# Kernel optimization log

Hardware: AMD Instinct MI355X
Metric: run time of the kernel (lower is better)

## Reference

```python
import jax, jax.numpy as jnp
import numpy as np

N_NODES = 100000
N_EDGES = 1600000
IN_CH = 128
HID = 128
OUT_CH = 16
N_GRAPHS = 64


def setup_inputs() -> dict:
    key = jax.random.key(0)
    ks = jax.random.split(key, 8)
    x = jax.random.normal(ks[0], (N_NODES, IN_CH), dtype=jnp.float32)
    edge_index = jax.random.randint(ks[1], (2, N_EDGES), 0, N_NODES, dtype=jnp.int64)
    batch = jnp.sort(jax.random.randint(ks[2], (N_NODES,), 0, N_GRAPHS, dtype=jnp.int64))
    s1 = 1.0 / np.sqrt(IN_CH)
    s2 = 1.0 / np.sqrt(HID)
    W1 = jax.random.uniform(ks[3], (IN_CH, HID), jnp.float32, -s1, s1)
    b1 = jnp.zeros((HID,), jnp.float32)
    W2 = jax.random.uniform(ks[4], (HID, HID), jnp.float32, -s2, s2)
    b2 = jnp.zeros((HID,), jnp.float32)
    Wfc = jax.random.uniform(ks[5], (HID, OUT_CH), jnp.float32, -s2, s2)
    bfc = jax.random.uniform(ks[6], (OUT_CH,), jnp.float32, -s2, s2)
    return {"x": x, "W1": W1, "b1": b1, "W2": W2, "b2": b2,
            "Wfc": Wfc, "bfc": bfc, "edge_index": edge_index, "batch": batch}


def _gcn_conv(x, W, b, src, dst, deg_inv_sqrt, deg_inv):
    # GCNConv with self-loops: out = D^-1/2 (A+I) D^-1/2 (x W) + b
    h = x @ W                                   # [N, H]
    norm = deg_inv_sqrt[src] * deg_inv_sqrt[dst]  # [E]
    agg = jax.ops.segment_sum(h[src] * norm[:, None], dst, num_segments=N_NODES)
    # self-loop term: deg_inv_sqrt[i]^2 * h[i]
    return agg + h * deg_inv[:, None] + b


def reference(x, W1, b1, W2, b2, Wfc, bfc, edge_index, batch):
    src, dst = edge_index[0], edge_index[1]
    # degree including self-loop
    deg = jax.ops.segment_sum(jnp.ones((N_EDGES,), jnp.float32), dst, num_segments=N_NODES) + 1.0
    deg_inv_sqrt = jax.lax.rsqrt(deg)
    deg_inv = 1.0 / deg
    h = jax.nn.relu(_gcn_conv(x, W1, b1, src, dst, deg_inv_sqrt, deg_inv))
    h = jax.nn.relu(_gcn_conv(h, W2, b2, src, dst, deg_inv_sqrt, deg_inv))
    # global mean pool over graphs
    sums = jax.ops.segment_sum(h, batch, num_segments=N_GRAPHS)          # [G, H]
    counts = jax.ops.segment_sum(jnp.ones((N_NODES,), jnp.float32), batch, num_segments=N_GRAPHS)
    pooled = sums / jnp.maximum(counts, 1.0)[:, None]
    return pooled @ Wfc + bfc
```

## Files before the change

### kernel.cpp

```cpp
#include <hip/hip_runtime.h>
#include <math.h>

#define NN 100000
#define NE 1600000
#define CH 128
#define OUTC 16
#define NG 64

#define CBSH 8
#define NCB 391
#define CHK 4096
#define HCHK 8192
#define HISTB 196
#define PREPB 391
#define MAXB 6144
#define PS 8
#define LDA 136

typedef __attribute__((ext_vector_type(8))) short bf16x8;
typedef __attribute__((ext_vector_type(4))) float f32x4;

__device__ __forceinline__ unsigned short f2bf(float f) {
    union { float f; unsigned u; } v; v.f = f;
    unsigned r = v.u + 0x7FFF + ((v.u >> 16) & 1);
    return (unsigned short)(r >> 16);
}
__device__ __forceinline__ float bflo(unsigned u) {
    union { unsigned u; float f; } v; v.u = u << 16; return v.f;
}
__device__ __forceinline__ float bfhi(unsigned u) {
    union { unsigned u; float f; } v; v.u = u & 0xffff0000u; return v.f;
}

__global__ __launch_bounds__(256) void k_fused0(const int* __restrict__ edst, int* __restrict__ bcnt,
                         const float* __restrict__ W2, unsigned short* __restrict__ wt2,
                         const int* __restrict__ batch, int* __restrict__ gptr,
                         int* __restrict__ gfill, float* __restrict__ pooled) {
    int b = blockIdx.x;
    int t = threadIdx.x;
    if (b < HISTB) {
        __shared__ int h[NCB];
        for (int i = t; i < NCB; i += 256) h[i] = 0;
        __syncthreads();
        int base = b * HCHK;
#pragma unroll
        for (int i = 0; i < 32; i++) {
            int e = base + i * 256 + t;
            if (e < NE) atomicAdd(&h[edst[e] >> CBSH], 1);
        }
        __syncthreads();
        for (int i = t; i < NCB; i += 256)
            if (h[i]) atomicAdd(&bcnt[i], h[i]);
    } else {
        int i = (b - HISTB) * 256 + t;
        if (i < CH * CH) {
            int k = i >> 7, n = i & 127;
            wt2[n * CH + k] = f2bf(W2[i]);
        }
        if (i < NCB) gfill[i] = 0;
        if (i < NG * CH) pooled[i] = 0.f;
        if (i < NN) {
            int bb = batch[i];
            int prev = (i == 0) ? -1 : batch[i - 1];
            for (int g = prev + 1; g <= bb; g++) gptr[g] = i;
            if (i == NN - 1) {
                for (int g = bb + 1; g <= NG; g++) gptr[g] = NN;
            }
        }
    }
}

__global__ __launch_bounds__(512) void k_passA(const int* __restrict__ src, const int* __restrict__ dst,
                        const int* __restrict__ bcnt, int* __restrict__ gfill,
                        unsigned* __restrict__ ebuf, int* __restrict__ ebase) {
    __shared__ unsigned lbuf[CHK];
    __shared__ unsigned short lbkt[CHK];
    __shared__ int hcnt[NCB];
    __shared__ int hbase[512];
    __shared__ int eb[512];
    __shared__ int goff[NCB];
    int t = threadIdx.x;
    for (int i = t; i < NCB; i += 512) hcnt[i] = 0;
    eb[t] = (t < NCB) ? bcnt[t] : 0;
    __syncthreads();
    int base = blockIdx.x * CHK;
    int cb[8], slot[8]; unsigned pk[8];
#pragma unroll
    for (int i = 0; i < 8; i++) {
        int e = base + i * 512 + t;
        cb[i] = -1;
        if (e < NE) {
            int d = dst[e], s = src[e];
            cb[i] = d >> CBSH;
            pk[i] = ((unsigned)s << CBSH) | (unsigned)(d & 255);
            slot[i] = atomicAdd(&hcnt[cb[i]], 1);
        }
    }
    __syncthreads();
    hbase[t] = (t < NCB) ? hcnt[t] : 0;
    __syncthreads();
    for (int off = 1; off < 512; off <<= 1) {
        int v1 = 0, v2 = 0;
        if (t >= off) { v1 = hbase[t - off]; v2 = eb[t - off]; }
        __syncthreads();
        if (t >= off) { hbase[t] += v1; eb[t] += v2; }
        __syncthreads();
    }
    if (t < NCB) {
        int c = hcnt[t];
        int g = c ? atomicAdd(&gfill[t], c) : 0;
        int eb_ex = t ? eb[t - 1] : 0;
        goff[t] = eb_ex + g - (hbase[t] - c);
    }
    if (blockIdx.x == 0) {
        if (t == 0) ebase[0] = 0;
        if (t < NCB) ebase[t + 1] = eb[t];
    }
    __syncthreads();
#pragma unroll
    for (int i = 0; i < 8; i++) {
        if (cb[i] >= 0) {
            int pos = hbase[cb[i]] - hcnt[cb[i]] + slot[i];
            lbuf[pos] = pk[i];
            lbkt[pos] = (unsigned short)cb[i];
        }
    }
    __syncthreads();
    int total = min(NE - base, CHK);
    for (int p = t; p < total; p += 512) {
        unsigned v = lbuf[p];
        int bk = lbkt[p];
        ebuf[goff[bk] + p] = v;
    }
}

__launch_bounds__(256, 2)
__global__ void k_fusedB(const unsigned* __restrict__ ebuf, const int* __restrict__ ebase,
                         int* __restrict__ degi, int* __restrict__ rowst,
                         float* __restrict__ dis, int* __restrict__ csr,
                         const float* __restrict__ x, const float* __restrict__ W1,
                         unsigned short* __restrict__ bufA) {
    __shared__ __align__(16) unsigned short smem[128 * LDA];
    int b = blockIdx.x;
    int t = threadIdx.x;

    if (b < NCB) {
        int* cnt   = (int*)smem;
        int* nbase = cnt + 256;
        int* fill  = nbase + 256;
        int* stage = fill + 256;
        int cb = b;
        int nb0 = cb << CBSH;
        int ncnt = min(256, NN - nb0);
        int e0 = ebase[cb], e1 = ebase[cb + 1];
        cnt[t] = 0; fill[t] = 0;
        __syncthreads();
        for (int e = e0 + t; e < e1; e += 256)
            atomicAdd(&cnt[ebuf[e] & 255], 1);
        __syncthreads();
        nbase[t] = cnt[t];
        __syncthreads();
        for (int off = 1; off < 256; off <<= 1) {
            int v = 0;
            if (t >= off) v = nbase[t - off];
            __syncthreads();
            if (t >= off) nbase[t] += v;
            __syncthreads();
        }
        for (int e = e0 + t; e < e1; e += 256) {
            unsigned v = ebuf[e];
            int local = v & 255;
            int s = atomicAdd(&fill[local], 1);
            stage[nbase[local] - cnt[local] + s] = (int)(v >> CBSH);
        }
        __syncthreads();
        int total = e1 - e0;
        for (int p = t; p < total; p += 256) csr[e0 + p] = stage[p];
        if (t < ncnt) {
            int c = cnt[t];
            degi[nb0 + t] = c;
            rowst[nb0 + t] = e0 + nbase[t] - c;
            dis[nb0 + t] = rsqrtf((float)c + 1.0f);
        }
    } else {
        unsigned short* wlds = smem;
#pragma unroll
        for (int it = 0; it < 64; it++) {
            int i = it * 256 + t;
            int k = i >> 7, n = i & 127;
            wlds[n * LDA + k] = f2bf(W1[i]);
        }
        __syncthreads();

        int wave = t >> 6, lane = t & 63;
        int quad = lane >> 4, l16 = lane & 15;
        int rbase = (b - NCB) * 128 + wave * 32;

        bf16x8 af[2][4];
#pragma unroll
        for (int s = 0; s < 2; s++) {
            int row = rbase + s * 16 + l16;
            if (row >= NN) row = NN - 1;
            const float* arow = x + (size_t)row * CH + quad * 8;
#pragma unroll
            for (int ks = 0; ks < 4; ks++) {
                float4 lo = *(const float4*)(arow + ks * 32);
                float4 hi = *(const float4*)(arow + ks * 32 + 4);
                union { bf16x8 v; unsigned short u[8]; } tmp;
                tmp.u[0] = f2bf(lo.x); tmp.u[1] = f2bf(lo.y);
                tmp.u[2] = f2bf(lo.z); tmp.u[3] = f2bf(lo.w);
                tmp.u[4] = f2bf(hi.x); tmp.u[5] = f2bf(hi.y);
                tmp.u[6] = f2bf(hi.z); tmp.u[7] = f2bf(hi.w);
                af[s][ks] = tmp.v;
            }
        }

        f32x4 acc[2][8];
#pragma unroll
        for (int s = 0; s < 2; s++)
#pragma unroll
            for (int tt = 0; tt < 8; tt++) acc[s][tt] = (f32x4){0.f, 0.f, 0.f, 0.f};

#pragma unroll
        for (int tt = 0; tt < 8; tt++) {
            const unsigned short* wcol = &wlds[(tt * 16 + l16) * LDA + quad * 8];
            bf16x8 b0 = *(const bf16x8*)(wcol);
            bf16x8 b1 = *(const bf16x8*)(wcol + 32);
            bf16x8 b2 = *(const bf16x8*)(wcol + 64);
            bf16x8 b3 = *(const bf16x8*)(wcol + 96);
#pragma unroll
            for (int s = 0; s < 2; s++) {
                acc[s][tt] = __builtin_amdgcn_mfma_f32_16x16x32_bf16(af[s][0], b0, acc[s][tt], 0, 0, 0);
                acc[s][tt] = __builtin_amdgcn_mfma_f32_16x16x32_bf16(af[s][1], b1, acc[s][tt], 0, 0, 0);
                acc[s][tt] = __builtin_amdgcn_mfma_f32_16x16x32_bf16(af[s][2], b2, acc[s][tt], 0, 0, 0);
                acc[s][tt] = __builtin_amdgcn_mfma_f32_16x16x32_bf16(af[s][3], b3, acc[s][tt], 0, 0, 0);
            }
        }

#pragma unroll
        for (int s = 0; s < 2; s++) {
#pragma unroll
            for (int r = 0; r < 4; r++) {
                int orow = rbase + s * 16 + quad * 4 + r;
                if (orow < NN) {
#pragma unroll
                    for (int tt = 0; tt < 8; tt++)
                        bufA[(size_t)orow * CH + tt * 16 + l16] = f2bf(acc[s][tt][r]);
                }
            }
        }
    }
}

__global__ __launch_bounds__(256) void k_agg_w(const unsigned short* __restrict__ ht, const int* __restrict__ rowst,
                      const int* __restrict__ degi, const int* __restrict__ csr,
                      const float* __restrict__ dis, const float* __restrict__ bias,
                      unsigned short* __restrict__ out) {
    int t = threadIdx.x;
    int grp = t >> 4;
    int q = t & 15;
    int n = blockIdx.x * 16 + grp;
    const uint4* base = (const uint4*)ht;

    float d = dis[n];
    uint4 sv = base[(size_t)n * 16 + q];
    float a[8];
    a[0] = d * bflo(sv.x); a[1] = d * bfhi(sv.x);
    a[2] = d * bflo(sv.y); a[3] = d * bfhi(sv.y);
    a[4] = d * bflo(sv.z); a[5] = d * bfhi(sv.z);
    a[6] = d * bflo(sv.w); a[7] = d * bfhi(sv.w);

    int start = rowst[n];
    int c = degi[n];
    int nb = c & ~7;
    int j = 0;
    for (; j < nb; j += 8) {
        int idx[8];
#pragma unroll
        for (int u = 0; u < 8; u++) idx[u] = csr[start + j + u];
        uint4 v[8]; float w[8];
#pragma unroll
        for (int u = 0; u < 8; u++) v[u] = base[(size_t)idx[u] * 16 + q];
#pragma unroll
        for (int u = 0; u < 8; u++) w[u] = dis[idx[u]];
#pragma unroll
        for (int u = 0; u < 8; u++) {
            a[0] = fmaf(w[u], bflo(v[u].x), a[0]); a[1] = fmaf(w[u], bfhi(v[u].x), a[1]);
            a[2] = fmaf(w[u], bflo(v[u].y), a[2]); a[3] = fmaf(w[u], bfhi(v[u].y), a[3]);
            a[4] = fmaf(w[u], bflo(v[u].z), a[4]); a[5] = fmaf(w[u], bfhi(v[u].z), a[5]);
            a[6] = fmaf(w[u], bflo(v[u].w), a[6]); a[7] = fmaf(w[u], bfhi(v[u].w), a[7]);
        }
    }
    if (j < c) {
        int idx[8];
#pragma unroll
        for (int u = 0; u < 8; u++) { int e = j + u; idx[u] = csr[start + (e < c ? e : c - 1)]; }
        uint4 v[8]; float w[8];
#pragma unroll
        for (int u = 0; u < 8; u++) v[u] = base[(size_t)idx[u] * 16 + q];
#pragma unroll
        for (int u = 0; u < 8; u++) w[u] = dis[idx[u]];
#pragma unroll
        for (int u = 0; u < 8; u++) {
            if (j + u < c) {
                a[0] = fmaf(w[u], bflo(v[u].x), a[0]); a[1] = fmaf(w[u], bfhi(v[u].x), a[1]);
                a[2] = fmaf(w[u], bflo(v[u].y), a[2]); a[3] = fmaf(w[u], bfhi(v[u].y), a[3]);
                a[4] = fmaf(w[u], bflo(v[u].z), a[4]); a[5] = fmaf(w[u], bfhi(v[u].z), a[5]);
                a[6] = fmaf(w[u], bflo(v[u].w), a[6]); a[7] = fmaf(w[u], bfhi(v[u].w), a[7]);
            }
        }
    }

    const float4* bp = (const float4*)bias;
    float4 b0 = bp[q * 2], b1 = bp[q * 2 + 1];
    uint4 o;
    {
        float ox = fmaxf(fmaf(d, a[0], b0.x), 0.f), oy = fmaxf(fmaf(d, a[1], b0.y), 0.f);
        o.x = ((unsigned)f2bf(oy) << 16) | (unsigned)f2bf(ox);
        ox = fmaxf(fmaf(d, a[2], b0.z), 0.f); oy = fmaxf(fmaf(d, a[3], b0.w), 0.f);
        o.y = ((unsigned)f2bf(oy) << 16) | (unsigned)f2bf(ox);
        ox = fmaxf(fmaf(d, a[4], b1.x), 0.f); oy = fmaxf(fmaf(d, a[5], b1.y), 0.f);
        o.z = ((unsigned)f2bf(oy) << 16) | (unsigned)f2bf(ox);
        ox = fmaxf(fmaf(d, a[6], b1.z), 0.f); oy = fmaxf(fmaf(d, a[7], b1.w), 0.f);
        o.w = ((unsigned)f2bf(oy) << 16) | (unsigned)f2bf(ox);
    }
    ((uint4*)out)[(size_t)n * 16 + q] = o;
}

__launch_bounds__(256, 2)
__global__ void k_gemm2(const unsigned short* __restrict__ Av,
                        const unsigned short* __restrict__ WT,
                        const float* __restrict__ dis,
                        unsigned short* __restrict__ out) {
    int tid = threadIdx.x;
    int wave = tid >> 6, lane = tid & 63;
    int quad = lane >> 4, l16 = lane & 15;

    int rbase = blockIdx.x * 128 + wave * 32;

    bf16x8 af[2][4];
#pragma unroll
    for (int s = 0; s < 2; s++) {
        int row = rbase + s * 16 + l16;
        if (row >= NN) row = NN - 1;
        const unsigned short* arow = Av + (size_t)row * CH + quad * 8;
#pragma unroll
        for (int ks = 0; ks < 4; ks++) af[s][ks] = *(const bf16x8*)(arow + ks * 32);
    }

    f32x4 acc[2][8];
#pragma unroll
    for (int s = 0; s < 2; s++)
#pragma unroll
        for (int t = 0; t < 8; t++) acc[s][t] = (f32x4){0.f, 0.f, 0.f, 0.f};

#pragma unroll
    for (int t = 0; t < 8; t++) {
        const unsigned short* wcol = WT + (size_t)(t * 16 + l16) * CH + quad * 8;
        bf16x8 b0 = *(const bf16x8*)(wcol);
        bf16x8 b1 = *(const bf16x8*)(wcol + 32);
        bf16x8 b2 = *(const bf16x8*)(wcol + 64);
        bf16x8 b3 = *(const bf16x8*)(wcol + 96);
#pragma unroll
        for (int s = 0; s < 2; s++) {
            acc[s][t] = __builtin_amdgcn_mfma_f32_16x16x32_bf16(af[s][0], b0, acc[s][t], 0, 0, 0);
            acc[s][t] = __builtin_amdgcn_mfma_f32_16x16x32_bf16(af[s][1], b1, acc[s][t], 0, 0, 0);
            acc[s][t] = __builtin_amdgcn_mfma_f32_16x16x32_bf16(af[s][2], b2, acc[s][t], 0, 0, 0);
            acc[s][t] = __builtin_amdgcn_mfma_f32_16x16x32_bf16(af[s][3], b3, acc[s][t], 0, 0, 0);
        }
    }

#pragma unroll
    for (int s = 0; s < 2; s++) {
#pragma unroll
        for (int r = 0; r < 4; r++) {
            int orow = rbase + s * 16 + quad * 4 + r;
            if (orow < NN) {
                float d = dis[orow];
#pragma unroll
                for (int t = 0; t < 8; t++) {
                    out[(size_t)orow * CH + t * 16 + l16] = f2bf(acc[s][t][r] * d);
                }
            }
        }
    }
}

__global__ __launch_bounds__(256) void k_agg(const unsigned short* __restrict__ ht, const int* __restrict__ rowst,
                      const int* __restrict__ degi, const int* __restrict__ csr,
                      const float* __restrict__ dis, const float* __restrict__ bias,
                      unsigned short* __restrict__ out) {
    int t = threadIdx.x;
    int grp = t >> 4;
    int q = t & 15;
    int n = blockIdx.x * 16 + grp;
    const uint4* base = (const uint4*)ht;

    uint4 sv = base[(size_t)n * 16 + q];
    float a[8];
    a[0] = bflo(sv.x); a[1] = bfhi(sv.x);
    a[2] = bflo(sv.y); a[3] = bfhi(sv.y);
    a[4] = bflo(sv.z); a[5] = bfhi(sv.z);
    a[6] = bflo(sv.w); a[7] = bfhi(sv.w);

    int start = rowst[n];
    int c = degi[n];
    int nb = c & ~7;
    int j = 0;
    for (; j < nb; j += 8) {
        int idx[8];
#pragma unroll
        for (int u = 0; u < 8; u++) idx[u] = csr[start + j + u];
        uint4 v[8];
#pragma unroll
        for (int u = 0; u < 8; u++) v[u] = base[(size_t)idx[u] * 16 + q];
#pragma unroll
        for (int u = 0; u < 8; u++) {
            a[0] += bflo(v[u].x); a[1] += bfhi(v[u].x);
            a[2] += bflo(v[u].y); a[3] += bfhi(v[u].y);
            a[4] += bflo(v[u].z); a[5] += bfhi(v[u].z);
            a[6] += bflo(v[u].w); a[7] += bfhi(v[u].w);
        }
    }
    if (j < c) {
        int idx[8];
#pragma unroll
        for (int u = 0; u < 8; u++) { int e = j + u; idx[u] = csr[start + (e < c ? e : c - 1)]; }
        uint4 v[8];
#pragma unroll
        for (int u = 0; u < 8; u++) v[u] = base[(size_t)idx[u] * 16 + q];
#pragma unroll
        for (int u = 0; u < 8; u++) {
            if (j + u < c) {
                a[0] += bflo(v[u].x); a[1] += bfhi(v[u].x);
                a[2] += bflo(v[u].y); a[3] += bfhi(v[u].y);
                a[4] += bflo(v[u].z); a[5] += bfhi(v[u].z);
                a[6] += bflo(v[u].w); a[7] += bfhi(v[u].w);
            }
        }
    }

    float d = dis[n];
    const float4* bp = (const float4*)bias;
    float4 b0 = bp[q * 2], b1 = bp[q * 2 + 1];
    uint4 o;
    {
        float ox = fmaxf(fmaf(d, a[0], b0.x), 0.f), oy = fmaxf(fmaf(d, a[1], b0.y), 0.f);
        o.x = ((unsigned)f2bf(oy) << 16) | (unsigned)f2bf(ox);
        ox = fmaxf(fmaf(d, a[2], b0.z), 0.f); oy = fmaxf(fmaf(d, a[3], b0.w), 0.f);
        o.y = ((unsigned)f2bf(oy) << 16) | (unsigned)f2bf(ox);
        ox = fmaxf(fmaf(d, a[4], b1.x), 0.f); oy = fmaxf(fmaf(d, a[5], b1.y), 0.f);
        o.z = ((unsigned)f2bf(oy) << 16) | (unsigned)f2bf(ox);
        ox = fmaxf(fmaf(d, a[6], b1.z), 0.f); oy = fmaxf(fmaf(d, a[7], b1.w), 0.f);
        o.w = ((unsigned)f2bf(oy) << 16) | (unsigned)f2bf(ox);
    }
    ((uint4*)out)[(size_t)n * 16 + q] = o;
}

__global__ __launch_bounds__(512) void k_pool2(const unsigned short* __restrict__ h,
                                               const int* __restrict__ gptr,
                                               float* __restrict__ pooled) {
    int g = blockIdx.x >> 3;
    int s = blockIdx.x & 7;
    int gs = gptr[g], ge = gptr[g + 1];
    int len = ge - gs;
    int i0 = gs + (int)(((long long)len * s) >> 3);
    int i1 = gs + (int)(((long long)len * (s + 1)) >> 3);
    int t = threadIdx.x;
    int pr = t & 63;
    int ro = t >> 6;
    const unsigned* base = (const unsigned*)h;
    float s0 = 0.f, s1 = 0.f;
    for (int n = i0 + ro; n < i1; n += 8) {
        unsigned v = base[(size_t)n * 64 + pr];
        s0 += bflo(v); s1 += bfhi(v);
    }
    __shared__ float red[2][8][64];
    red[0][ro][pr] = s0; red[1][ro][pr] = s1;
    __syncthreads();
    for (int off = 4; off >= 1; off >>= 1) {
        if (ro < off) {
            red[0][ro][pr] += red[0][ro + off][pr];
            red[1][ro][pr] += red[1][ro + off][pr];
        }
        __syncthreads();
    }
    if (ro == 0) {
        atomicAdd(&pooled[g * CH + pr * 2],     red[0][0][pr]);
        atomicAdd(&pooled[g * CH + pr * 2 + 1], red[1][0][pr]);
    }
}

__global__ void k_final(const float* __restrict__ pooled, const int* __restrict__ gptr,
                        const float* __restrict__ Wfc, const float* __restrict__ bfc,
                        float* __restrict__ out) {
    int idx = blockIdx.x * 256 + threadIdx.x;
    if (idx >= NG * OUTC) return;
    int g = idx >> 4, o = idx & 15;
    float c = (float)(gptr[g + 1] - gptr[g]);
    float inv = 1.0f / fmaxf(c, 1.0f);
    float s = 0.f;
    for (int k = 0; k < CH; k++) s += pooled[g * CH + k] * Wfc[k * OUTC + o];
    out[idx] = fmaf(s, inv, bfc[o]);
}

extern "C" void kernel_launch(void* const* d_in, const int* in_sizes, int n_in,
                              void* d_out, int out_size, void* d_ws, size_t ws_size,
                              hipStream_t stream) {
    (void)in_sizes; (void)n_in; (void)out_size; (void)ws_size;
    const float* x   = (const float*)d_in[0];
    const float* W1  = (const float*)d_in[1];
    const float* b1  = (const float*)d_in[2];
    const float* W2  = (const float*)d_in[3];
    const float* b2  = (const float*)d_in[4];
    const float* Wfc = (const float*)d_in[5];
    const float* bfc = (const float*)d_in[6];
    const int* ei    = (const int*)d_in[7];
    const int* batch = (const int*)d_in[8];
    const int* esrc = ei;
    const int* edst = ei + NE;
    float* out = (float*)d_out;

    char* w = (char*)d_ws;
    unsigned short* bufA = (unsigned short*)w; w += (size_t)NN * CH * 2;
    unsigned short* bufB = (unsigned short*)w; w += (size_t)NN * CH * 2;
    unsigned short* wt2  = (unsigned short*)w; w += (size_t)CH * CH * 2;
    unsigned* ebuf = (unsigned*)w; w += (size_t)NE * 4;
    int* csr    = (int*)w;    w += (size_t)NE * 4;
    int* degi   = (int*)w;    w += (size_t)NN * 4;
    int* rowst  = (int*)w;    w += (size_t)NN * 4;
    float* dis  = (float*)w;  w += (size_t)NN * 4;
    int* bcnt   = (int*)w;    w += NCB * 4;
    int* ebase  = (int*)w;    w += (NCB + 1) * 4;
    int* gfill  = (int*)w;    w += NCB * 4;
    int* gptr   = (int*)w;    w += (NG + 1) * 4;
    float* pooled = (float*)w; w += (size_t)NG * CH * 4;

    const int gemmBlocks = (NN + 127) / 128;
    const int aggBlocks  = NN / 16;
    const int passABlocks = (NE + CHK - 1) / CHK;

    hipMemsetAsync(bcnt, 0, NCB * sizeof(int), stream);

    k_fused0<<<HISTB + PREPB, 256, 0, stream>>>(edst, bcnt, W2, wt2, batch, gptr, gfill, pooled);
    k_passA<<<passABlocks, 512, 0, stream>>>(esrc, edst, bcnt, gfill, ebuf, ebase);
    k_fusedB<<<NCB + gemmBlocks, 256, 0, stream>>>(ebuf, ebase, degi, rowst, dis, csr, x, W1, bufA);

    k_agg_w<<<aggBlocks, 256, 0, stream>>>(bufA, rowst, degi, csr, dis, b1, bufB);
    k_gemm2<<<gemmBlocks, 256, 0, stream>>>(bufB, wt2, dis, bufA);
    k_agg<<<aggBlocks, 256, 0, stream>>>(bufA, rowst, degi, csr, dis, b2, bufB);

    k_pool2<<<NG * PS, 512, 0, stream>>>(bufB, gptr, pooled);
    k_final<<<(NG * OUTC + 255) / 256, 256, 0, stream>>>(pooled, gptr, Wfc, bfc, out);
}
```

Measured before the change: 312.9 us.

## Transpose MFMA operands for packed GEMM stores and fuse final FC into pool

The two GEMM kernels swap the MFMA A/B operands so each lane holds four consecutive output columns of one node. This lets the epilogue write packed 8-byte bf16 stores instead of scattered 2-byte stores. Separately, the pooling kernel now counts finished blocks with an atomic counter, and the last block computes the final FC layer. That removes one kernel launch, at the cost of a large shared-memory array in every pooling block and a threadfence/atomic handshake.

```diff
diff --git a/kernel.cpp b/kernel.cpp
--- a/kernel.cpp
+++ b/kernel.cpp
@@ -35,7 +35,8 @@
 __global__ __launch_bounds__(256) void k_fused0(const int* __restrict__ edst, int* __restrict__ bcnt,
                          const float* __restrict__ W2, unsigned short* __restrict__ wt2,
                          const int* __restrict__ batch, int* __restrict__ gptr,
-                         int* __restrict__ gfill, float* __restrict__ pooled) {
+                         int* __restrict__ gfill, float* __restrict__ pooled,
+                         int* __restrict__ done) {
     int b = blockIdx.x;
     int t = threadIdx.x;
     if (b < HISTB) {
@@ -59,6 +60,7 @@
         }
         if (i < NCB) gfill[i] = 0;
         if (i < NG * CH) pooled[i] = 0.f;
+        if (i == 0) *done = 0;
         if (i < NN) {
             int bb = batch[i];
             int prev = (i == 0) ? -1 : batch[i - 1];
@@ -230,22 +232,23 @@
             bf16x8 b3 = *(const bf16x8*)(wcol + 96);
 #pragma unroll
             for (int s = 0; s < 2; s++) {
-                acc[s][tt] = __builtin_amdgcn_mfma_f32_16x16x32_bf16(af[s][0], b0, acc[s][tt], 0, 0, 0);
-                acc[s][tt] = __builtin_amdgcn_mfma_f32_16x16x32_bf16(af[s][1], b1, acc[s][tt], 0, 0, 0);
-                acc[s][tt] = __builtin_amdgcn_mfma_f32_16x16x32_bf16(af[s][2], b2, acc[s][tt], 0, 0, 0);
-                acc[s][tt] = __builtin_amdgcn_mfma_f32_16x16x32_bf16(af[s][3], b3, acc[s][tt], 0, 0, 0);
+                acc[s][tt] = __builtin_amdgcn_mfma_f32_16x16x32_bf16(b0, af[s][0], acc[s][tt], 0, 0, 0);
+                acc[s][tt] = __builtin_amdgcn_mfma_f32_16x16x32_bf16(b1, af[s][1], acc[s][tt], 0, 0, 0);
+                acc[s][tt] = __builtin_amdgcn_mfma_f32_16x16x32_bf16(b2, af[s][2], acc[s][tt], 0, 0, 0);
+                acc[s][tt] = __builtin_amdgcn_mfma_f32_16x16x32_bf16(b3, af[s][3], acc[s][tt], 0, 0, 0);
             }
         }
 
 #pragma unroll
         for (int s = 0; s < 2; s++) {
-#pragma unroll
-            for (int r = 0; r < 4; r++) {
-                int orow = rbase + s * 16 + quad * 4 + r;
-                if (orow < NN) {
-#pragma unroll
-                    for (int tt = 0; tt < 8; tt++)
-                        bufA[(size_t)orow * CH + tt * 16 + l16] = f2bf(acc[s][tt][r]);
+            int node = rbase + s * 16 + l16;
+            if (node < NN) {
+#pragma unroll
+                for (int tt = 0; tt < 8; tt++) {
+                    unsigned lo = ((unsigned)f2bf(acc[s][tt][1]) << 16) | (unsigned)f2bf(acc[s][tt][0]);
+                    unsigned hi = ((unsigned)f2bf(acc[s][tt][3]) << 16) | (unsigned)f2bf(acc[s][tt][2]);
+                    uint2 pk; pk.x = lo; pk.y = hi;
+                    *(uint2*)(bufA + (size_t)node * CH + tt * 16 + quad * 4) = pk;
                 }
             }
         }
@@ -363,24 +366,25 @@
         bf16x8 b3 = *(const bf16x8*)(wcol + 96);
 #pragma unroll
         for (int s = 0; s < 2; s++) {
-            acc[s][t] = __builtin_amdgcn_mfma_f32_16x16x32_bf16(af[s][0], b0, acc[s][t], 0, 0, 0);
-            acc[s][t] = __builtin_amdgcn_mfma_f32_16x16x32_bf16(af[s][1], b1, acc[s][t], 0, 0, 0);
-            acc[s][t] = __builtin_amdgcn_mfma_f32_16x16x32_bf16(af[s][2], b2, acc[s][t], 0, 0, 0);
-            acc[s][t] = __builtin_amdgcn_mfma_f32_16x16x32_bf16(af[s][3], b3, acc[s][t], 0, 0, 0);
+            acc[s][t] = __builtin_amdgcn_mfma_f32_16x16x32_bf16(b0, af[s][0], acc[s][t], 0, 0, 0);
+            acc[s][t] = __builtin_amdgcn_mfma_f32_16x16x32_bf16(b1, af[s][1], acc[s][t], 0, 0, 0);
+            acc[s][t] = __builtin_amdgcn_mfma_f32_16x16x32_bf16(b2, af[s][2], acc[s][t], 0, 0, 0);
+            acc[s][t] = __builtin_amdgcn_mfma_f32_16x16x32_bf16(b3, af[s][3], acc[s][t], 0, 0, 0);
         }
     }
 
 #pragma unroll
     for (int s = 0; s < 2; s++) {
-#pragma unroll
-        for (int r = 0; r < 4; r++) {
-            int orow = rbase + s * 16 + quad * 4 + r;
-            if (orow < NN) {
-                float d = dis[orow];
-#pragma unroll
-                for (int t = 0; t < 8; t++) {
-                    out[(size_t)orow * CH + t * 16 + l16] = f2bf(acc[s][t][r] * d);
-                }
+        int node = rbase + s * 16 + l16;
+        int cl = (node < NN) ? node : NN - 1;
+        float d = dis[cl];
+        if (node < NN) {
+#pragma unroll
+            for (int t = 0; t < 8; t++) {
+                unsigned lo = ((unsigned)f2bf(acc[s][t][1] * d) << 16) | (unsigned)f2bf(acc[s][t][0] * d);
+                unsigned hi = ((unsigned)f2bf(acc[s][t][3] * d) << 16) | (unsigned)f2bf(acc[s][t][2] * d);
+                uint2 pk; pk.x = lo; pk.y = hi;
+                *(uint2*)(out + (size_t)node * CH + t * 16 + quad * 4) = pk;
             }
         }
     }
@@ -457,9 +461,13 @@
     ((uint4*)out)[(size_t)n * 16 + q] = o;
 }
 
-__global__ __launch_bounds__(512) void k_pool2(const unsigned short* __restrict__ h,
+__global__ __launch_bounds__(512) void k_pool_final(const unsigned short* __restrict__ h,
                                                const int* __restrict__ gptr,
-                                               float* __restrict__ pooled) {
+                                               float* __restrict__ pooled,
+                                               int* __restrict__ done,
+                                               const float* __restrict__ Wfc,
+                                               const float* __restrict__ bfc,
+                                               float* __restrict__ out) {
     int g = blockIdx.x >> 3;
     int s = blockIdx.x & 7;
     int gs = gptr[g], ge = gptr[g + 1];
@@ -489,19 +497,27 @@
         atomicAdd(&pooled[g * CH + pr * 2],     red[0][0][pr]);
         atomicAdd(&pooled[g * CH + pr * 2 + 1], red[1][0][pr]);
     }
-}
-
-__global__ void k_final(const float* __restrict__ pooled, const int* __restrict__ gptr,
-                        const float* __restrict__ Wfc, const float* __restrict__ bfc,
-                        float* __restrict__ out) {
-    int idx = blockIdx.x * 256 + threadIdx.x;
-    if (idx >= NG * OUTC) return;
-    int g = idx >> 4, o = idx & 15;
-    float c = (float)(gptr[g + 1] - gptr[g]);
-    float inv = 1.0f / fmaxf(c, 1.0f);
-    float s = 0.f;
-    for (int k = 0; k < CH; k++) s += pooled[g * CH + k] * Wfc[k * OUTC + o];
-    out[idx] = fmaf(s, inv, bfc[o]);
+
+    __shared__ int lastFlag;
+    __shared__ float plds[NG * CH];
+    __syncthreads();
+    if (t == 0) {
+        __threadfence();
+        int r = atomicAdd(done, 1);
+        lastFlag = (r == NG * PS - 1) ? 1 : 0;
+    }
+    __syncthreads();
+    if (!lastFlag) return;
+    for (int i = t; i < NG * CH; i += 512) plds[i] = atomicAdd(&pooled[i], 0.0f);
+    __syncthreads();
+    for (int idx = t; idx < NG * OUTC; idx += 512) {
+        int gg = idx >> 4, o = idx & 15;
+        float c = (float)(gptr[gg + 1] - gptr[gg]);
+        float inv = 1.0f / fmaxf(c, 1.0f);
+        float acc = 0.f;
+        for (int k = 0; k < CH; k++) acc += plds[gg * CH + k] * Wfc[k * OUTC + o];
+        out[idx] = fmaf(acc, inv, bfc[o]);
+    }
 }
 
 extern "C" void kernel_launch(void* const* d_in, const int* in_sizes, int n_in,
@@ -535,6 +551,7 @@
     int* gfill  = (int*)w;    w += NCB * 4;
     int* gptr   = (int*)w;    w += (NG + 1) * 4;
     float* pooled = (float*)w; w += (size_t)NG * CH * 4;
+    int* done   = (int*)w;    w += 4;
 
     const int gemmBlocks = (NN + 127) / 128;
     const int aggBlocks  = NN / 16;
@@ -542,7 +559,7 @@
 
     hipMemsetAsync(bcnt, 0, NCB * sizeof(int), stream);
 
-    k_fused0<<<HISTB + PREPB, 256, 0, stream>>>(edst, bcnt, W2, wt2, batch, gptr, gfill, pooled);
+    k_fused0<<<HISTB + PREPB, 256, 0, stream>>>(edst, bcnt, W2, wt2, batch, gptr, gfill, pooled, done);
     k_passA<<<passABlocks, 512, 0, stream>>>(esrc, edst, bcnt, gfill, ebuf, ebase);
     k_fusedB<<<NCB + gemmBlocks, 256, 0, stream>>>(ebuf, ebase, degi, rowst, dis, csr, x, W1, bufA);
 
@@ -550,6 +567,5 @@
     k_gemm2<<<gemmBlocks, 256, 0, stream>>>(bufB, wt2, dis, bufA);
     k_agg<<<aggBlocks, 256, 0, stream>>>(bufA, rowst, degi, csr, dis, b2, bufB);
 
-    k_pool2<<<NG * PS, 512, 0, stream>>>(bufB, gptr, pooled);
-    k_final<<<(NG * OUTC + 255) / 256, 256, 0, stream>>>(pooled, gptr, Wfc, bfc, out);
-}
+    k_pool_final<<<NG * PS, 512, 0, stream>>>(bufB, gptr, pooled, done, Wfc, bfc, out);
+}
```

Result: slower. 329.5 us (+5.3%).
